# Performance work log

Measured on AMD Instinct MI355X. Metric: run time of the kernel, lower is better.

The kernel has to match this reference:

```python
import math
import jax, jax.numpy as jnp
import numpy as np

TOP_K = 16
LOW_FREQ = 1
MAX_SEL = 32


def setup_inputs() -> dict:
    key = jax.random.key(0)
    x = jax.random.normal(key, (32, 2048, 512), dtype=jnp.float32)
    return {"x": x}


def reference(x):
    # x: (B, T, D)
    B, T, D = x.shape
    dtype = x.dtype

    xf = jnp.fft.rfft(x, axis=1)  # (B, T//2+1, D) complex
    f_full = jnp.fft.rfftfreq(T, d=1.0).astype(dtype)
    if T % 2 == 0:
        xf = xf[:, LOW_FREQ:-1, :]
        f_vec = f_full[LOW_FREQ:-1]
    else:
        xf = xf[:, LOW_FREQ:, :]
        f_vec = f_full[LOW_FREQ:]
    Lf = xf.shape[1]
    K = min(TOP_K, Lf)

    # top-k over frequency axis, per (b, d)
    xf_t = jnp.transpose(xf, (0, 2, 1))  # (B, D, Lf)
    _, idx = jax.lax.top_k(jnp.abs(xf_t), K)  # (B, D, K), sorted descending
    idx = idx[:, :, : min(MAX_SEL, K)]
    Ksel = idx.shape[2]

    x_sel = jnp.take_along_axis(xf_t, idx, axis=2)  # (B, D, Ksel) complex
    f_sel = f_vec[idx]                               # (B, D, Ksel)
    amp = jnp.abs(x_sel).astype(dtype)
    ph = jnp.angle(x_sel).astype(dtype)

    # y[b,t,d] = sum_k amp * cos(2*pi*f*t + phase), t = linspace(0,1,T)
    two_pi_t = (2.0 * math.pi) * jnp.linspace(0.0, 1.0, T, dtype=dtype)  # (T,)

    def step(acc, kin):
        a, f, p = kin  # each (B, D)
        acc = acc + a[..., None] * jnp.cos(f[..., None] * two_pi_t + p[..., None])
        return acc, None

    init = jnp.zeros((B, D, T), dtype)
    ks = (jnp.moveaxis(amp, 2, 0), jnp.moveaxis(f_sel, 2, 0), jnp.moveaxis(ph, 2, 0))
    y_bdt, _ = jax.lax.scan(step, init, ks)
    return jnp.transpose(y_bdt, (0, 2, 1))  # (B, T, D)
```

## Files before the change

### kernel.cpp

```cpp
#include <hip/hip_runtime.h>
#include <math.h>

#ifndef M_PI
#define M_PI 3.14159265358979323846
#endif

constexpr int cB = 32;
constexpr int cT = 2048;
constexpr int cD = 512;
constexpr int cK = 16;
constexpr int TCH = 64;

__device__ __forceinline__ int PZ(int i) { return i + (i >> 4); }

__device__ __forceinline__ float2 twLO(const float2* TW, int e) {
  return TW[PZ(e)];
}
__device__ __forceinline__ float2 twHI(const float2* TW, int e) {
  float2 w = TW[PZ(e - 512)];
  return make_float2(w.y, -w.x);
}
__device__ __forceinline__ float2 twDYN(const float2* TW, int e) {
  float2 w = TW[PZ(e & 511)];
  return (e < 512) ? w : make_float2(w.y, -w.x);
}

template <int S>
__device__ __forceinline__ void pass8(float2* Z, const float2* TW, int B0, int O) {
  float vr[8], vi[8];
#pragma unroll
  for (int m = 0; m < 8; ++m) {
    const float2 z = Z[PZ(B0 + S * m)];
    vr[m] = z.x; vi[m] = z.y;
  }
  constexpr int E1 = 1024 / (4 * S);
  constexpr int E2 = 1024 / (2 * S);
  constexpr int E3 = 1024 / S;
#pragma unroll
  for (int m = 0; m < 4; ++m) {
    const int e = (O + S * m) * E1;
    const float2 w = (m < 2) ? twLO(TW, e) : twHI(TW, e);
    const float ar = vr[m], ai = vi[m], br = vr[m + 4], bi = vi[m + 4];
    vr[m] = ar + br; vi[m] = ai + bi;
    const float tr = ar - br, ti = ai - bi;
    vr[m + 4] = tr * w.x - ti * w.y; vi[m + 4] = tr * w.y + ti * w.x;
  }
#pragma unroll
  for (int q = 0; q < 8; q += 4) {
#pragma unroll
    for (int m2 = 0; m2 < 2; ++m2) {
      const int m = q + m2;
      const int e = (O + S * m2) * E2;
      const float2 w = (m2 == 0) ? twLO(TW, e) : twHI(TW, e);
      const float ar = vr[m], ai = vi[m], br = vr[m + 2], bi = vi[m + 2];
      vr[m] = ar + br; vi[m] = ai + bi;
      const float tr = ar - br, ti = ai - bi;
      vr[m + 2] = tr * w.x - ti * w.y; vi[m + 2] = tr * w.y + ti * w.x;
    }
  }
  {
    const int e = O * E3;
    const float2 w = (S == 1) ? twLO(TW, 0) : twDYN(TW, e);
#pragma unroll
    for (int m = 0; m < 8; m += 2) {
      const float ar = vr[m], ai = vi[m], br = vr[m + 1], bi = vi[m + 1];
      vr[m] = ar + br; vi[m] = ai + bi;
      const float tr = ar - br, ti = ai - bi;
      vr[m + 1] = tr * w.x - ti * w.y; vi[m + 1] = tr * w.y + ti * w.x;
    }
  }
#pragma unroll
  for (int m = 0; m < 8; ++m) Z[PZ(B0 + S * m)] = make_float2(vr[m], vi[m]);
}

__global__ __launch_bounds__(256) void k_fft_topk(const float* __restrict__ x,
                                                  float* __restrict__ amp_out,
                                                  float* __restrict__ kf_out,
                                                  float* __restrict__ ph_out) {
  __shared__ float2 Z[2176];
  __shared__ float2 TW[544];
  __shared__ float  CV[128];
  __shared__ int    CK[128];
  __shared__ int    CC[4];

  const int tid   = threadIdx.x;
  const int lane  = tid & 63;
  const int wave  = tid >> 6;

  const int i_  = blockIdx.x;
  const int c_  = i_ & 7;
  const int j_  = i_ >> 3;
  const int G_  = c_ * 64 + (j_ >> 4);
  const int s_  = j_ & 15;
  const int b     = G_ >> 4;
  const int dpair = ((G_ & 15) << 4) | s_;
  const int d0    = dpair * 2;

  const float2* xp = (const float2*)x + (size_t)b * cT * (cD / 2) + dpair;
  float2 vv[8];
#pragma unroll
  for (int u = 0; u < 8; ++u) {
    vv[u] = xp[(size_t)(tid + 256 * u) * (cD / 2)];
  }

  for (int j = tid; j < 512; j += 256) {
    float s, c;
    __sincosf(-2.0f * (float)M_PI * (float)j * (1.0f / 2048.0f), &s, &c);
    TW[PZ(j)] = make_float2(c, s);
  }
#pragma unroll
  for (int u = 0; u < 8; ++u) {
    Z[PZ(tid + 256 * u)] = vv[u];
  }
  __syncthreads();

#pragma unroll
  for (int u = 0; u < 2; ++u) {
    const int O = tid + 256 * u;
    float vr[4], vi[4];
#pragma unroll
    for (int m = 0; m < 4; ++m) {
      const float2 z = Z[PZ(O + 512 * m)];
      vr[m] = z.x; vi[m] = z.y;
    }
#pragma unroll
    for (int m = 0; m < 2; ++m) {
      const float2 w = (m == 0) ? twLO(TW, O) : twHI(TW, O + 512);
      const float ar = vr[m], ai = vi[m], br = vr[m + 2], bi = vi[m + 2];
      vr[m] = ar + br; vi[m] = ai + bi;
      const float tr = ar - br, ti = ai - bi;
      vr[m + 2] = tr * w.x - ti * w.y; vi[m + 2] = tr * w.y + ti * w.x;
    }
    {
      const float2 w = (u == 0) ? twLO(TW, 2 * O) : twHI(TW, 2 * O);
#pragma unroll
      for (int m = 0; m < 4; m += 2) {
        const float ar = vr[m], ai = vi[m], br = vr[m + 1], bi = vi[m + 1];
        vr[m] = ar + br; vi[m] = ai + bi;
        const float tr = ar - br, ti = ai - bi;
        vr[m + 1] = tr * w.x - ti * w.y; vi[m + 1] = tr * w.y + ti * w.x;
      }
    }
#pragma unroll
    for (int m = 0; m < 4; ++m) Z[PZ(O + 512 * m)] = make_float2(vr[m], vi[m]);
  }
  __syncthreads();

  pass8<64>(Z, TW, (tid >> 6) * 512 + (tid & 63), tid & 63);
  __syncthreads();
  pass8<8>(Z, TW, (tid >> 3) * 64 + (tid & 7), tid & 7);
  __syncthreads();
  pass8<1>(Z, TW, tid * 8, 0);
  __syncthreads();

  const int col  = wave >> 1;
  const int half = wave & 1;
  float v[8];
  int   kk[8];
#pragma unroll
  for (int u = 0; u < 8; ++u) {
    const int k = half * 512 + lane + 64 * u;
    kk[u] = k;
    if (k == 0) { v[u] = -1.0f; continue; }
    const float2 p = Z[PZ((int)(__brev((unsigned)k) >> 21))];
    const float2 q = Z[PZ((int)(__brev((unsigned)(2048 - k)) >> 21))];
    float xr, xi;
    if (col == 0) { xr = p.x + q.x; xi = p.y - q.y; }
    else          { xr = p.y + q.y; xi = q.x - p.x; }
    v[u] = xr * xr + xi * xi;
  }

  {
    float lm = v[0];
#pragma unroll
    for (int j = 1; j < 8; ++j) lm = fmaxf(lm, v[j]);
    float sm = lm;
#pragma unroll
    for (int k2 = 2; k2 <= 64; k2 <<= 1) {
#pragma unroll
      for (int j = k2 >> 1; j > 0; j >>= 1) {
        const float om = __shfl_xor(sm, j);
        const bool wmin = ((lane & k2) == 0) != ((lane & j) == 0);
        const bool oless = (om < sm);
        sm = (oless == wmin) ? om : sm;
      }
    }
    const float thr = __shfl(sm, 16);

    unsigned long long mball[8];
    int cnt = 0;
#pragma unroll
    for (int j = 0; j < 8; ++j) {
      mball[j] = __ballot(v[j] >= thr);
      cnt += __popcll(mball[j]);
    }

    if (cnt <= 32) {
      int pos = 0;
#pragma unroll
      for (int j = 0; j < 8; ++j) {
        const int p = pos + __popcll(mball[j] & ((1ull << lane) - 1ull));
        if (v[j] >= thr) { CV[wave * 32 + p] = v[j]; CK[wave * 32 + p] = kk[j]; }
        pos += __popcll(mball[j]);
      }
      if (lane == 0) CC[wave] = cnt;
    } else {
      float fv[8];
#pragma unroll
      for (int j = 0; j < 8; ++j) fv[j] = v[j];
      for (int it = 0; it < cK + 1; ++it) {
        float bv = fv[0]; int bj = 0;
#pragma unroll
        for (int j = 1; j < 8; ++j) if (fv[j] > bv) { bv = fv[j]; bj = j; }
        int bk = kk[bj];
        for (int off = 32; off > 0; off >>= 1) {
          const float ov = __shfl_down(bv, off);
          const int   ok = __shfl_down(bk, off);
          if (ov > bv) { bv = ov; bk = ok; }
        }
        const int   bkb = __shfl(bk, 0);
        const float bvb = __shfl(bv, 0);
#pragma unroll
        for (int j = 0; j < 8; ++j) if (kk[j] == bkb) fv[j] = -1.0f;
        if (lane == 0) { CV[wave * 32 + it] = bvb; CK[wave * 32 + it] = bkb; }
      }
      if (lane == 0) CC[wave] = cK + 1;
    }
  }
  __syncthreads();

  if ((wave & 1) == 0) {
    const int c0 = CC[wave];
    const int c1 = CC[wave + 1];
    const int n  = c0 + c1;
    float mv = -1.0f;
    int   mk = 5000 + lane;
    if (lane < c0)     { mv = CV[wave * 32 + lane];            mk = CK[wave * 32 + lane]; }
    else if (lane < n) { mv = CV[(wave + 1) * 32 + lane - c0]; mk = CK[(wave + 1) * 32 + lane - c0]; }

#pragma unroll
    for (int k2 = 2; k2 <= 64; k2 <<= 1) {
#pragma unroll
      for (int j = k2 >> 1; j > 0; j >>= 1) {
        const float ov = __shfl_xor(mv, j);
        const int   ok = __shfl_xor(mk, j);
        const bool wmin  = ((lane & k2) == 0) != ((lane & j) == 0);
        const bool oless = (ov < mv) || (ov == mv && ok > mk);
        if (oless == wmin) { mv = ov; mk = ok; }
      }
    }
    const float myv = mv;
    const int   myk = mk;

    const float v15 = __shfl(myv, 15);
    const float v16 = __shfl(myv, 16);
    const int   k15 = __shfl(myk, 15);
    const int   k16 = __shfl(myk, 16);
    bool  do_swap = false;
    double aR = 0.0, pR = 0.0;
    if (v15 - v16 < 1e-3f * v15) {
      const float* colp = x + (size_t)b * cT * cD + (d0 + col);
      double m2[2], XR[2], XI[2];
      for (int bb = 0; bb < 2; ++bb) {
        const int k = bb ? k16 : k15;
        double sr = 0.0, si = 0.0;
        for (int u = 0; u < 32; ++u) {
          const int t = lane + 64 * u;
          const int m = (k * t) & 2047;
          double s, c;
          sincos(-M_PI * (double)m / 1024.0, &s, &c);
          const double xv = (double)colp[(size_t)t * cD];
          sr += xv * c; si += xv * s;
        }
        for (int off = 32; off > 0; off >>= 1) {
          sr += __shfl_down(sr, off);
          si += __shfl_down(si, off);
        }
        sr = __shfl(sr, 0); si = __shfl(si, 0);
        m2[bb] = sr * sr + si * si; XR[bb] = sr; XI[bb] = si;
      }
      if (m2[1] > m2[0]) {
        do_swap = true;
        aR = sqrt(m2[1]);
        pR = atan2(XI[1], XR[1]);
      }
    }

    if (lane < cK) {
      float a, p, kf;
      if (do_swap && lane == 15) {
        a = (float)aR; p = (float)pR; kf = (float)k16;
      } else {
        const int k = myk;
        const float2 zp = Z[PZ((int)(__brev((unsigned)k) >> 21))];
        const float2 zq = Z[PZ((int)(__brev((unsigned)(2048 - k)) >> 21))];
        float xr, xi;
        if (col == 0) { xr = 0.5f * (zp.x + zq.x); xi = 0.5f * (zp.y - zq.y); }
        else          { xr = 0.5f * (zp.y + zq.y); xi = 0.5f * (zq.x - zp.x); }
        a = sqrtf(xr * xr + xi * xi);
        p = atan2f(xi, xr);
        kf = (float)k;
      }
      const size_t cidx = ((size_t)b * cD + (d0 + col)) * cK + lane;
      amp_out[cidx] = a;
      kf_out[cidx]  = kf;
      ph_out[cidx]  = p;
    }
  }
}

__global__ __launch_bounds__(256) void k_recon(const float* __restrict__ amp_in,
                                               const float* __restrict__ kf_in,
                                               const float* __restrict__ ph_in,
                                               float* __restrict__ y) {
  const int tid = threadIdx.x;
  const int d   = blockIdx.y * 256 + tid;
  const int b   = blockIdx.z;
  const int t0  = blockIdx.x * TCH;
  const size_t cidx = ((size_t)b * cD + d) * cK;
  const float Cw = (float)(2.0 * M_PI / (2047.0 * 2048.0));
  const float t0f = (float)t0;

  float amp[cK], kf[cK], ph[cK];
#pragma unroll
  for (int q = 0; q < 4; ++q) {
    const float4 va = ((const float4*)(amp_in + cidx))[q];
    const float4 vk = ((const float4*)(kf_in + cidx))[q];
    const float4 vp = ((const float4*)(ph_in + cidx))[q];
    amp[4*q+0] = va.x; amp[4*q+1] = va.y; amp[4*q+2] = va.z; amp[4*q+3] = va.w;
    kf [4*q+0] = vk.x; kf [4*q+1] = vk.y; kf [4*q+2] = vk.z; kf [4*q+3] = vk.w;
    ph [4*q+0] = vp.x; ph [4*q+1] = vp.y; ph [4*q+2] = vp.z; ph [4*q+3] = vp.w;
  }

  float r[cK], dd[cK], cm[cK];
  float acc0 = 0.0f, acc1 = 0.0f;
#pragma unroll
  for (int j = 0; j < cK; ++j) {
    const float w  = kf[j] * Cw;
    const float w2 = w * w;
    cm[j] = w2 - w2 * w2 * (1.0f / 12.0f);
    const float kt = kf[j] * t0f;
    const float r0 = amp[j] * __cosf(__fmaf_rn(kt, Cw, ph[j]));
    const float r1 = amp[j] * __cosf(__fmaf_rn(kt + kf[j], Cw, ph[j]));
    r[j] = r1; dd[j] = r1 - r0;
    acc0 += r0; acc1 += r1;
  }
  float* yp = y + ((size_t)b * cT + t0) * cD + d;
  yp[0] = acc0;
  yp[cD] = acc1;
  yp += 2 * (size_t)cD;
#pragma unroll 2
  for (int t = 2; t < TCH; ++t) {
    float acc = 0.0f;
#pragma unroll
    for (int j = 0; j < cK; ++j) {
      dd[j] = __fmaf_rn(-cm[j], r[j], dd[j]);
      r[j] += dd[j];
      acc += r[j];
    }
    *yp = acc;
    yp += cD;
  }
}

extern "C" void kernel_launch(void* const* d_in, const int* in_sizes, int n_in,
                              void* d_out, int out_size, void* d_ws, size_t ws_size,
                              hipStream_t stream) {
  const float* x = (const float*)d_in[0];
  float* out = (float*)d_out;

  float* amp = (float*)d_ws;
  float* kf  = amp + (size_t)cB * cD * cK;
  float* ph  = kf + (size_t)cB * cD * cK;

  k_fft_topk<<<cB * cD / 2, 256, 0, stream>>>(x, amp, kf, ph);

  dim3 g3(cT / TCH, cD / 256, cB), b3(256, 1, 1);
  k_recon<<<g3, b3, 0, stream>>>(amp, kf, ph, out);
}
```

Before: 334.5 us.

## Fuse FFT/top-k and reconstruction into one kernel; do first FFT stages in registers

Merges the top-k FFT kernel and the reconstruction kernel into a single kernel. The selected amplitude, frequency and phase values now stay in shared memory instead of going through a global workspace. Each block writes the full output for its pair of d columns, and each thread uses a Chebyshev recurrence over 8 time points spaced 256 apart. The first two radix-2 FFT stages are done directly in registers with sincos twiddles, which removes one shared-memory round trip and a barrier. The cost is that each thread's output stores are strided by d-pair, giving 8-byte writes per row, and reconstruction parallelism is now tied to the FFT grid.

```diff
diff --git a/kernel.cpp b/kernel.cpp
--- a/kernel.cpp
+++ b/kernel.cpp
@@ -9,7 +9,6 @@
 constexpr int cT = 2048;
 constexpr int cD = 512;
 constexpr int cK = 16;
-constexpr int TCH = 64;
 
 __device__ __forceinline__ int PZ(int i) { return i + (i >> 4); }
 
@@ -23,6 +22,13 @@
 __device__ __forceinline__ float2 twDYN(const float2* TW, int e) {
   float2 w = TW[PZ(e & 511)];
   return (e < 512) ? w : make_float2(w.y, -w.x);
+}
+
+__device__ __forceinline__ void bfly(float2& a, float2& b, float wx, float wy) {
+  const float tr = a.x - b.x, ti = a.y - b.y;
+  a.x += b.x; a.y += b.y;
+  b.x = tr * wx - ti * wy;
+  b.y = tr * wy + ti * wx;
 }
 
 template <int S>
@@ -73,15 +79,15 @@
   for (int m = 0; m < 8; ++m) Z[PZ(B0 + S * m)] = make_float2(vr[m], vi[m]);
 }
 
-__global__ __launch_bounds__(256) void k_fft_topk(const float* __restrict__ x,
-                                                  float* __restrict__ amp_out,
-                                                  float* __restrict__ kf_out,
-                                                  float* __restrict__ ph_out) {
+__global__ __launch_bounds__(256) void k_fused(const float* __restrict__ x,
+                                               float* __restrict__ y) {
   __shared__ float2 Z[2176];
   __shared__ float2 TW[544];
-  __shared__ float  CV[128];
+  __shared__ float4 CVq[32];
   __shared__ int    CK[128];
   __shared__ int    CC[4];
+  float* CV = (float*)CVq;
+  float4* PRM = CVq;
 
   const int tid   = threadIdx.x;
   const int lane  = tid & 63;
@@ -108,41 +114,21 @@
     __sincosf(-2.0f * (float)M_PI * (float)j * (1.0f / 2048.0f), &s, &c);
     TW[PZ(j)] = make_float2(c, s);
   }
-#pragma unroll
-  for (int u = 0; u < 8; ++u) {
-    Z[PZ(tid + 256 * u)] = vv[u];
-  }
-  __syncthreads();
 
 #pragma unroll
   for (int u = 0; u < 2; ++u) {
     const int O = tid + 256 * u;
-    float vr[4], vi[4];
-#pragma unroll
-    for (int m = 0; m < 4; ++m) {
-      const float2 z = Z[PZ(O + 512 * m)];
-      vr[m] = z.x; vi[m] = z.y;
-    }
-#pragma unroll
-    for (int m = 0; m < 2; ++m) {
-      const float2 w = (m == 0) ? twLO(TW, O) : twHI(TW, O + 512);
-      const float ar = vr[m], ai = vi[m], br = vr[m + 2], bi = vi[m + 2];
-      vr[m] = ar + br; vi[m] = ai + bi;
-      const float tr = ar - br, ti = ai - bi;
-      vr[m + 2] = tr * w.x - ti * w.y; vi[m + 2] = tr * w.y + ti * w.x;
-    }
-    {
-      const float2 w = (u == 0) ? twLO(TW, 2 * O) : twHI(TW, 2 * O);
-#pragma unroll
-      for (int m = 0; m < 4; m += 2) {
-        const float ar = vr[m], ai = vi[m], br = vr[m + 1], bi = vi[m + 1];
-        vr[m] = ar + br; vi[m] = ai + bi;
-        const float tr = ar - br, ti = ai - bi;
-        vr[m + 1] = tr * w.x - ti * w.y; vi[m + 1] = tr * w.y + ti * w.x;
-      }
-    }
-#pragma unroll
-    for (int m = 0; m < 4; ++m) Z[PZ(O + 512 * m)] = make_float2(vr[m], vi[m]);
+    float s1, c1, s2, c2;
+    __sincosf(-2.0f * (float)M_PI * (float)O * (1.0f / 2048.0f), &s1, &c1);
+    __sincosf(-2.0f * (float)M_PI * (float)(2 * O) * (1.0f / 2048.0f), &s2, &c2);
+    bfly(vv[u],     vv[u + 4], c1, s1);
+    bfly(vv[u + 2], vv[u + 6], s1, -c1);
+    bfly(vv[u],     vv[u + 2], c2, s2);
+    bfly(vv[u + 4], vv[u + 6], c2, s2);
+    Z[PZ(O)]        = vv[u];
+    Z[PZ(O + 512)]  = vv[u + 2];
+    Z[PZ(O + 1024)] = vv[u + 4];
+    Z[PZ(O + 1536)] = vv[u + 6];
   }
   __syncthreads();
 
@@ -301,65 +287,45 @@
         p = atan2f(xi, xr);
         kf = (float)k;
       }
-      const size_t cidx = ((size_t)b * cD + (d0 + col)) * cK + lane;
-      amp_out[cidx] = a;
-      kf_out[cidx]  = kf;
-      ph_out[cidx]  = p;
-    }
-  }
-}
-
-__global__ __launch_bounds__(256) void k_recon(const float* __restrict__ amp_in,
-                                               const float* __restrict__ kf_in,
-                                               const float* __restrict__ ph_in,
-                                               float* __restrict__ y) {
-  const int tid = threadIdx.x;
-  const int d   = blockIdx.y * 256 + tid;
-  const int b   = blockIdx.z;
-  const int t0  = blockIdx.x * TCH;
-  const size_t cidx = ((size_t)b * cD + d) * cK;
-  const float Cw = (float)(2.0 * M_PI / (2047.0 * 2048.0));
-  const float t0f = (float)t0;
-
-  float amp[cK], kf[cK], ph[cK];
-#pragma unroll
-  for (int q = 0; q < 4; ++q) {
-    const float4 va = ((const float4*)(amp_in + cidx))[q];
-    const float4 vk = ((const float4*)(kf_in + cidx))[q];
-    const float4 vp = ((const float4*)(ph_in + cidx))[q];
-    amp[4*q+0] = va.x; amp[4*q+1] = va.y; amp[4*q+2] = va.z; amp[4*q+3] = va.w;
-    kf [4*q+0] = vk.x; kf [4*q+1] = vk.y; kf [4*q+2] = vk.z; kf [4*q+3] = vk.w;
-    ph [4*q+0] = vp.x; ph [4*q+1] = vp.y; ph [4*q+2] = vp.z; ph [4*q+3] = vp.w;
-  }
-
-  float r[cK], dd[cK], cm[cK];
-  float acc0 = 0.0f, acc1 = 0.0f;
-#pragma unroll
-  for (int j = 0; j < cK; ++j) {
-    const float w  = kf[j] * Cw;
-    const float w2 = w * w;
-    cm[j] = w2 - w2 * w2 * (1.0f / 12.0f);
-    const float kt = kf[j] * t0f;
-    const float r0 = amp[j] * __cosf(__fmaf_rn(kt, Cw, ph[j]));
-    const float r1 = amp[j] * __cosf(__fmaf_rn(kt + kf[j], Cw, ph[j]));
-    r[j] = r1; dd[j] = r1 - r0;
-    acc0 += r0; acc1 += r1;
-  }
-  float* yp = y + ((size_t)b * cT + t0) * cD + d;
-  yp[0] = acc0;
-  yp[cD] = acc1;
-  yp += 2 * (size_t)cD;
-#pragma unroll 2
-  for (int t = 2; t < TCH; ++t) {
-    float acc = 0.0f;
-#pragma unroll
-    for (int j = 0; j < cK; ++j) {
-      dd[j] = __fmaf_rn(-cm[j], r[j], dd[j]);
-      r[j] += dd[j];
-      acc += r[j];
-    }
-    *yp = acc;
-    yp += cD;
+      PRM[col * cK + lane] = make_float4(a, kf, p, 0.0f);
+    }
+  }
+  __syncthreads();
+
+  {
+    const float Cw = (float)(2.0 * M_PI / (2047.0 * 2048.0));
+    const float tf = (float)tid;
+    float accA[8], accB[8];
+#pragma unroll
+    for (int n = 0; n < 8; ++n) { accA[n] = 0.0f; accB[n] = 0.0f; }
+
+#define RECON_COL(ACC, CBASE)                                              \
+    _Pragma("unroll")                                                      \
+    for (int j = 0; j < cK; ++j) {                                         \
+      const float4 pr = PRM[(CBASE) + j];                                  \
+      const float aj = pr.x, kj = pr.y, pj = pr.z;                         \
+      const float kt0  = kj * tf;                       \
+      const float k256 = kj * 256.0f;                   \
+      float y0 = aj * __cosf(__fmaf_rn(kt0, Cw, pj));                      \
+      float y1 = aj * __cosf(__fmaf_rn(kt0 + k256, Cw, pj));               \
+      const float cm2 = 2.0f * __cosf(k256 * Cw);                          \
+      ACC[0] += y0; ACC[1] += y1;                                          \
+      _Pragma("unroll")                                                    \
+      for (int n = 2; n < 8; ++n) {                                        \
+        const float y2 = __fmaf_rn(cm2, y1, -y0);                          \
+        ACC[n] += y2; y0 = y1; y1 = y2;                                    \
+      }                                                                    \
+    }
+
+    RECON_COL(accA, 0)
+    RECON_COL(accB, cK)
+#undef RECON_COL
+
+    float2* yp = (float2*)y + ((size_t)b * cT + tid) * (cD / 2) + dpair;
+#pragma unroll
+    for (int n = 0; n < 8; ++n) {
+      yp[(size_t)(256 * n) * (cD / 2)] = make_float2(accA[n], accB[n]);
+    }
   }
 }
 
@@ -368,13 +334,7 @@
                               hipStream_t stream) {
   const float* x = (const float*)d_in[0];
   float* out = (float*)d_out;
-
-  float* amp = (float*)d_ws;
-  float* kf  = amp + (size_t)cB * cD * cK;
-  float* ph  = kf + (size_t)cB * cD * cK;
-
-  k_fft_topk<<<cB * cD / 2, 256, 0, stream>>>(x, amp, kf, ph);
-
-  dim3 g3(cT / TCH, cD / 256, cB), b3(256, 1, 1);
-  k_recon<<<g3, b3, 0, stream>>>(amp, kf, ph, out);
-}
+  (void)d_ws; (void)ws_size;
+
+  k_fused<<<cB * cD / 2, 256, 0, stream>>>(x, out);
+}
```

After: 408.5 us. +22.1%, slower.

## Do first FFT stages in registers and replace block barriers with wave fences

Applied to the files above, without the earlier changes.

The first radix-4 stage now runs directly on the values loaded from global memory. This removes one LDS store, a block barrier and an LDS reload, and the twiddles for that stage come from inline sincos. The barriers between the three radix-8 passes become wave-local LDS waits plus a scheduling barrier, because each wave only touches its own 512-element slice in those passes. This relies on that wave-local data ownership holding exactly; if it breaks, the results go wrong.

```diff
diff --git a/kernel.cpp b/kernel.cpp
--- a/kernel.cpp
+++ b/kernel.cpp
@@ -23,6 +23,18 @@
 __device__ __forceinline__ float2 twDYN(const float2* TW, int e) {
   float2 w = TW[PZ(e & 511)];
   return (e < 512) ? w : make_float2(w.y, -w.x);
+}
+
+__device__ __forceinline__ void bfly(float2& a, float2& b, float wx, float wy) {
+  const float tr = a.x - b.x, ti = a.y - b.y;
+  a.x += b.x; a.y += b.y;
+  b.x = tr * wx - ti * wy;
+  b.y = tr * wy + ti * wx;
+}
+
+__device__ __forceinline__ void wave_lds_fence() {
+  asm volatile("s_waitcnt lgkmcnt(0)" ::: "memory");
+  __builtin_amdgcn_sched_barrier(0);
 }
 
 template <int S>
@@ -108,48 +120,28 @@
     __sincosf(-2.0f * (float)M_PI * (float)j * (1.0f / 2048.0f), &s, &c);
     TW[PZ(j)] = make_float2(c, s);
   }
-#pragma unroll
-  for (int u = 0; u < 8; ++u) {
-    Z[PZ(tid + 256 * u)] = vv[u];
-  }
-  __syncthreads();
 
 #pragma unroll
   for (int u = 0; u < 2; ++u) {
     const int O = tid + 256 * u;
-    float vr[4], vi[4];
-#pragma unroll
-    for (int m = 0; m < 4; ++m) {
-      const float2 z = Z[PZ(O + 512 * m)];
-      vr[m] = z.x; vi[m] = z.y;
-    }
-#pragma unroll
-    for (int m = 0; m < 2; ++m) {
-      const float2 w = (m == 0) ? twLO(TW, O) : twHI(TW, O + 512);
-      const float ar = vr[m], ai = vi[m], br = vr[m + 2], bi = vi[m + 2];
-      vr[m] = ar + br; vi[m] = ai + bi;
-      const float tr = ar - br, ti = ai - bi;
-      vr[m + 2] = tr * w.x - ti * w.y; vi[m + 2] = tr * w.y + ti * w.x;
-    }
-    {
-      const float2 w = (u == 0) ? twLO(TW, 2 * O) : twHI(TW, 2 * O);
-#pragma unroll
-      for (int m = 0; m < 4; m += 2) {
-        const float ar = vr[m], ai = vi[m], br = vr[m + 1], bi = vi[m + 1];
-        vr[m] = ar + br; vi[m] = ai + bi;
-        const float tr = ar - br, ti = ai - bi;
-        vr[m + 1] = tr * w.x - ti * w.y; vi[m + 1] = tr * w.y + ti * w.x;
-      }
-    }
-#pragma unroll
-    for (int m = 0; m < 4; ++m) Z[PZ(O + 512 * m)] = make_float2(vr[m], vi[m]);
+    float s1, c1, s2, c2;
+    __sincosf(-2.0f * (float)M_PI * (float)O * (1.0f / 2048.0f), &s1, &c1);
+    __sincosf(-2.0f * (float)M_PI * (float)(2 * O) * (1.0f / 2048.0f), &s2, &c2);
+    bfly(vv[u],     vv[u + 4], c1, s1);
+    bfly(vv[u + 2], vv[u + 6], s1, -c1);
+    bfly(vv[u],     vv[u + 2], c2, s2);
+    bfly(vv[u + 4], vv[u + 6], c2, s2);
+    Z[PZ(O)]        = vv[u];
+    Z[PZ(O + 512)]  = vv[u + 2];
+    Z[PZ(O + 1024)] = vv[u + 4];
+    Z[PZ(O + 1536)] = vv[u + 6];
   }
   __syncthreads();
 
   pass8<64>(Z, TW, (tid >> 6) * 512 + (tid & 63), tid & 63);
-  __syncthreads();
+  wave_lds_fence();
   pass8<8>(Z, TW, (tid >> 3) * 64 + (tid & 7), tid & 7);
-  __syncthreads();
+  wave_lds_fence();
   pass8<1>(Z, TW, tid * 8, 0);
   __syncthreads();
 
```

New measurement: 334.0 us. No clear change (-0.1%).
